# Kernel tuning notes

Hardware: AMD Instinct MI355X
Metric: run time of the kernel (lower is better)

The kernel has to match this reference:

```python
import jax, jax.numpy as jnp
import numpy as np

D_MODEL = 1024
H = 16
D_K = D_MODEL // H
D_FF = 4096
EPS = 1e-6
NEG = -1e9


def setup_inputs() -> dict:
    key = jax.random.key(0)
    ks = jax.random.split(key, 8)
    B, S = 2, 2048
    src = jax.random.normal(ks[0], (B, S, D_MODEL), dtype=jnp.float32)
    src_mask = jnp.ones((B, 1, 1, S), dtype=jnp.int32)
    sc = 1.0 / np.sqrt(D_MODEL)
    wq = jax.random.normal(ks[1], (D_MODEL, D_MODEL), jnp.float32) * sc
    wk = jax.random.normal(ks[2], (D_MODEL, D_MODEL), jnp.float32) * sc
    wv = jax.random.normal(ks[3], (D_MODEL, D_MODEL), jnp.float32) * sc
    wo = jax.random.normal(ks[4], (D_MODEL, D_MODEL), jnp.float32) * sc
    w1 = jax.random.normal(ks[5], (D_FF, D_MODEL), jnp.float32) * sc
    b1 = jnp.zeros((D_FF,), jnp.float32)
    w2 = jax.random.normal(ks[6], (D_MODEL, D_FF), jnp.float32) * (1.0 / np.sqrt(D_FF))
    b2 = jnp.zeros((D_MODEL,), jnp.float32)
    a1 = jnp.ones((1,), jnp.float32)
    be1 = jnp.zeros((1,), jnp.float32)
    a2 = jnp.ones((1,), jnp.float32)
    be2 = jnp.zeros((1,), jnp.float32)
    return dict(src=src, src_mask=src_mask, wq=wq, wk=wk, wv=wv, wo=wo,
                w1=w1, b1=b1, w2=w2, b2=b2, a1=a1, be1=be1, a2=a2, be2=be2)


def layer_norm(x, alpha, bias):
    # torch: mean + unbiased std (ddof=1), eps added to std
    mean = jnp.mean(x, axis=-1, keepdims=True)
    std = jnp.sqrt(jnp.var(x, axis=-1, keepdims=True, ddof=1))
    return alpha * (x - mean) / (std + EPS) + bias


def mha(x, mask, wq, wk, wv, wo):
    B, S, _ = x.shape
    def split(t):  # [B,S,D] -> [B,H,S,D_K]
        return t.reshape(B, S, H, D_K).transpose(0, 2, 1, 3)
    q = split(x @ wq.T)
    k = split(x @ wk.T)
    v = split(x @ wv.T)
    scores = jnp.einsum('bhqd,bhkd->bhqk', q, k) / np.sqrt(D_K)
    scores = jnp.where(mask == 0, NEG, scores)
    attn = jax.nn.softmax(scores, axis=-1)
    out = jnp.einsum('bhqk,bhkd->bhqd', attn, v)
    out = out.transpose(0, 2, 1, 3).reshape(B, S, D_MODEL)
    return out @ wo.T


def reference(src, src_mask, wq, wk, wv, wo, w1, b1, w2, b2, a1, be1, a2, be2):
    x = layer_norm(src, a1, be1)
    src = src + mha(x, src_mask, wq, wk, wv, wo)
    x = layer_norm(src, a2, be2)
    ff = jax.nn.relu(x @ w1.T + b1) @ w2.T + b2
    return src + ff
```

## Files before the change

### kernel.cpp

```cpp
#include <hip/hip_runtime.h>
#include <hip/hip_bf16.h>

typedef unsigned short u16;
typedef unsigned int u32;
typedef float floatx4 __attribute__((ext_vector_type(4)));
typedef __bf16 bf16x8 __attribute__((ext_vector_type(8)));
typedef u16 ushort4v __attribute__((ext_vector_type(4)));
typedef u16 ushort8v __attribute__((ext_vector_type(8)));
typedef u32 u32x2 __attribute__((ext_vector_type(2)));

#define DEVI static __device__ __forceinline__

DEVI u16 f2bf(float f) {
    u32 u = __builtin_bit_cast(u32, f);
    u += 0x7fffu + ((u >> 16) & 1u);
    return (u16)(u >> 16);
}
DEVI float bf2f(u16 h) { return __builtin_bit_cast(float, (u32)h << 16); }

DEVI float fexp2(float x) { return __builtin_amdgcn_exp2f(x); }

DEVI u32 cvtpk_bf16(float lo, float hi) {
    u32 r;
    asm("v_cvt_pk_bf16_f32 %0, %1, %2" : "=v"(r) : "v"(lo), "v"(hi));
    return r;
}

DEVI void async_cp16(const u16* g, u16* l) {
    __builtin_amdgcn_global_load_lds((const __attribute__((address_space(1))) u32*)g,
                                     (__attribute__((address_space(3))) u32*)l, 16, 0, 0);
}

template<int N> DEVI void wait_vmcnt() {
    if constexpr (N == 0)      asm volatile("s_waitcnt vmcnt(0)" ::: "memory");
    else if constexpr (N == 2) asm volatile("s_waitcnt vmcnt(2)" ::: "memory");
    else if constexpr (N == 3) asm volatile("s_waitcnt vmcnt(3)" ::: "memory");
    else if constexpr (N == 4) asm volatile("s_waitcnt vmcnt(4)" ::: "memory");
    else if constexpr (N == 6) asm volatile("s_waitcnt vmcnt(6)" ::: "memory");
    else static_assert(N == 0, "add vmcnt case");
}

#define PH_BAR() asm volatile("s_barrier" ::: "memory")

DEVI void xcd_swizzle(int& bx, int& by, int gx, int gy) {
    int L = by * gx + bx;
    int xcd = L & 7, s = L >> 3;
    int gh = gy >> 2, xh = gx >> 1;
    int mg = xcd & 3, ng = xcd >> 2;
    by = mg * gh + s % gh;
    bx = ng * xh + s / gh;
}

template<int BM, int BN, int RW, int CW, bool QKV3, int NSPLIT, bool XSWZ,
         bool BIAS, bool RELU, bool RESID, bool OBF16, bool VTW>
__global__ __launch_bounds__(256) void gemm_nt(
    const u16* __restrict__ A,
    const u16* __restrict__ W0, const u16* __restrict__ W1, const u16* __restrict__ W2,
    const float* __restrict__ bias, const float* __restrict__ resid,
    void* __restrict__ o0, void* __restrict__ o1, void* __restrict__ o2,
    void* __restrict__ o3, int K, int lda, int Nper, int NX)
{
    static_assert(RW * CW == 4, "4 waves");
    constexpr int WM = BM / RW, WN = BN / CW;
    constexpr int MI = WM / 16, NI = WN / 16;
    constexpr int LPT = BM / 64 + BN / 64;
    constexpr int ASZ = 3 * BM * 32;
    constexpr int BSZ = 3 * BN * 32;
    __shared__ __align__(16) u16 smem[ASZ + BSZ];
    u16* Asm = smem;
    u16* Bsm = smem + ASZ;
    const int tid = threadIdx.x;
    const int w = tid >> 6, lane = tid & 63;
    const int q = lane >> 4, ml = lane & 15;
    const int wr = w / CW, wc = w % CW;
    int bx = blockIdx.x, by = blockIdx.y;
    if (XSWZ) xcd_swizzle(bx, by, gridDim.x, gridDim.y);
    const int m0 = by * BM;
    size_t kbase = 0;
    const u16* W = W0;
    void* outp = o0;
    if (NSPLIT > 1) {
        int part = bx / NX; bx -= part * NX; kbase = (size_t)part * K;
        outp = (part == 0) ? o0 : (part == 1 ? o1 : (part == 2 ? o2 : o3));
    }
    int n0 = bx * BN;
    bool vwrite = false;
    if (QKV3) {
        int sel = n0 / Nper;
        n0 -= sel * Nper;
        W = (sel == 0) ? W0 : (sel == 1 ? W1 : W2);
        outp = (sel == 0) ? o0 : (sel == 1 ? o1 : o2);
        if (VTW) vwrite = (sel == 2);
    }

    auto stage = [&](int buf, int kt) {
#pragma unroll
        for (int p = 0; p < BM / 64; ++p) {
            int g = p * 256 + tid;
            int r = g >> 2, s = g & 3;
            int c = s ^ ((r >> 1) & 3);
            async_cp16(A + (size_t)(m0 + r) * lda + kbase + kt + c * 8,
                       &Asm[buf * (BM * 32) + (p * 256 + w * 64) * 8]);
        }
#pragma unroll
        for (int p = 0; p < BN / 64; ++p) {
            int g = p * 256 + tid;
            int r = g >> 2, s = g & 3;
            int c = s ^ ((r >> 1) & 3);
            async_cp16(W + (size_t)(n0 + r) * lda + kbase + kt + c * 8,
                       &Bsm[buf * (BN * 32) + (p * 256 + w * 64) * 8]);
        }
    };

    const floatx4 fzero = {0.f, 0.f, 0.f, 0.f};
    floatx4 acc[MI][NI];
#pragma unroll
    for (int i = 0; i < MI; ++i)
#pragma unroll
        for (int j = 0; j < NI; ++j) acc[i][j] = fzero;

    const int nt = K >> 5;
    stage(0, 0);
    stage(1, 32);
    int cb = 0, nb = 2;
    for (int it = 0, kt = 0; it < nt; ++it, kt += 32) {
        wait_vmcnt<LPT>();
        __builtin_amdgcn_s_barrier();
        __builtin_amdgcn_sched_barrier(0);
        int ktn = kt + 64; if (ktn > K - 32) ktn = K - 32;
        stage(nb, ktn);
        __builtin_amdgcn_sched_barrier(0);
        const u16* Asb = &Asm[cb * (BM * 32)];
        const u16* Bsb = &Bsm[cb * (BN * 32)];
        bf16x8 af[MI], bfr[NI];
#pragma unroll
        for (int i = 0; i < MI; ++i) {
            int rm = wr * WM + i * 16 + ml;
            int s = q ^ ((rm >> 1) & 3);
            af[i] = *(const bf16x8*)&Asb[(rm * 4 + s) * 8];
        }
#pragma unroll
        for (int j = 0; j < NI; ++j) {
            int rn = wc * WN + j * 16 + ml;
            int s = q ^ ((rn >> 1) & 3);
            bfr[j] = *(const bf16x8*)&Bsb[(rn * 4 + s) * 8];
        }
#pragma unroll
        for (int i = 0; i < MI; ++i)
#pragma unroll
            for (int j = 0; j < NI; ++j)
                acc[i][j] = __builtin_amdgcn_mfma_f32_16x16x32_bf16(af[i], bfr[j], acc[i][j], 0, 0, 0);
        cb = cb == 2 ? 0 : cb + 1;
        nb = nb == 2 ? 0 : nb + 1;
    }

    wait_vmcnt<0>();

    if constexpr (OBF16) {
        __builtin_amdgcn_s_barrier();
        char* T = (char*)smem;
        if (VTW && vwrite) {
#pragma unroll
            for (int j = 0; j < NI; ++j) {
                int nl = wc * WN + j * 16 + ml;
#pragma unroll
                for (int i = 0; i < MI; ++i) {
                    int m4 = wr * WM + i * 16 + q * 4;
                    u32x2 pk = {(u32)f2bf(acc[i][j][0]) | ((u32)f2bf(acc[i][j][1]) << 16),
                                (u32)f2bf(acc[i][j][2]) | ((u32)f2bf(acc[i][j][3]) << 16)};
                    *(u32x2*)(T + nl * (BM * 2) + ((m4 * 2) ^ ((nl & 15) << 4))) = pk;
                }
            }
            __syncthreads();
            const int bb = m0 >> 11, sres = m0 & 2047;
            constexpr int CPR = BM / 8, RPP = 256 / CPR;
#pragma unroll
            for (int p = 0; p < BN / RPP; ++p) {
                int nr = p * RPP + (tid / CPR);
                int c0 = (tid % CPR) * 8;
                bf16x8 vv = *(const bf16x8*)(T + nr * (BM * 2) + ((c0 * 2) ^ ((nr & 15) << 4)));
                *(bf16x8*)&((u16*)o3)[(size_t)(bb * 1024 + n0 + nr) * 2048 + sres + c0] = vv;
            }
        } else {
#pragma unroll
            for (int j = 0; j < NI; ++j) {
                int col = wc * WN + j * 16 + ml;
                float bj = 0.f;
                if (BIAS) bj = bias[n0 + col];
#pragma unroll
                for (int i = 0; i < MI; ++i) {
#pragma unroll
                    for (int r = 0; r < 4; ++r) {
                        int row = wr * WM + i * 16 + q * 4 + r;
                        float v = acc[i][j][r] + bj;
                        if (RELU) v = fmaxf(v, 0.f);
                        *(u16*)(T + row * (BN * 2) + ((col * 2) ^ ((row & 15) << 4))) = f2bf(v);
                    }
                }
            }
            __syncthreads();
            constexpr int CPR = BN / 8, RPP = 256 / CPR;
#pragma unroll
            for (int p = 0; p < BM / RPP; ++p) {
                int rr = p * RPP + (tid / CPR);
                int c0 = (tid % CPR) * 8;
                bf16x8 vv = *(const bf16x8*)(T + rr * (BN * 2) + ((c0 * 2) ^ ((rr & 15) << 4)));
                *(bf16x8*)&((u16*)outp)[(size_t)(m0 + rr) * Nper + n0 + c0] = vv;
            }
        }
    } else {
#pragma unroll
        for (int j = 0; j < NI; ++j) {
            int gn = n0 + wc * WN + j * 16 + ml;
            float bj = 0.f;
            if (BIAS) bj = bias[gn];
#pragma unroll
            for (int i = 0; i < MI; ++i) {
                int gm0 = m0 + wr * WM + i * 16 + q * 4;
#pragma unroll
                for (int r = 0; r < 4; ++r) {
                    size_t idx = (size_t)(gm0 + r) * Nper + gn;
                    float v = acc[i][j][r] + bj;
                    if (RELU) v = fmaxf(v, 0.f);
                    if (RESID) v += resid[idx];
                    ((float*)outp)[idx] = v;
                }
            }
        }
    }
}

template<bool QKV3, int NSPLIT, bool BIAS, bool RELU, bool VTW>
__global__ __launch_bounds__(512, 2) void gemm8p(
    const u16* __restrict__ A,
    const u16* __restrict__ W0, const u16* __restrict__ W1, const u16* __restrict__ W2,
    const float* __restrict__ bias,
    void* __restrict__ o0, void* __restrict__ o1, void* __restrict__ o2,
    void* __restrict__ o3, int K, int lda, int Nper, int NX)
{
    __shared__ __align__(16) u16 smem[65536];
    u16* Asm = smem;
    u16* Bsm = smem + 32768;
    const int tid = threadIdx.x;
    const int w = tid >> 6, lane = tid & 63;
    const int q = lane >> 4, ml = lane & 15;
    const int wr = w >> 2, wc = w & 3;
    int bx = blockIdx.x, by = blockIdx.y;
    xcd_swizzle(bx, by, gridDim.x, gridDim.y);
    const int m0 = by * 256;
    size_t kbase = 0;
    const u16* W = W0;
    void* outp = o0;
    if (NSPLIT > 1) {
        int part = bx / NX; bx -= part * NX; kbase = (size_t)part * K;
        outp = (part == 0) ? o0 : (part == 1 ? o1 : (part == 2 ? o2 : o3));
    }
    int n0 = bx * 256;
    if (QKV3) {
        int sel = n0 / Nper; n0 -= sel * Nper;
        W = (sel == 0) ? W0 : (sel == 1 ? W1 : W2);
        outp = (sel == 0) ? o0 : (sel == 1 ? o1 : o2);
    }

    auto stA = [&](int d, int kh, int kt) {
#pragma unroll
        for (int p = 0; p < 2; ++p) {
            int c = p * 512 + tid;
            int r = c >> 2;
            int sc = (c & 3) ^ ((r >> 1) & 3);
            async_cp16(A + (size_t)(m0 + r) * lda + kbase + kt + kh * 32 + sc * 8,
                       &Asm[(d * 2 + kh) * 8192 + (p * 512 + w * 64) * 8]);
        }
    };
    auto stB = [&](int d, int kh, int kt) {
#pragma unroll
        for (int p = 0; p < 2; ++p) {
            int c = p * 512 + tid;
            int r = c >> 2;
            int sc = (c & 3) ^ ((r >> 1) & 3);
            async_cp16(W + (size_t)(n0 + r) * lda + kbase + kt + kh * 32 + sc * 8,
                       &Bsm[(d * 2 + kh) * 8192 + (p * 512 + w * 64) * 8]);
        }
    };
    auto rdA = [&](int d, int kh, int i) -> bf16x8 {
        int rm = wr * 128 + i * 16 + ml;
        return *(const bf16x8*)&Asm[(d * 2 + kh) * 8192 + (rm * 4 + (q ^ ((rm >> 1) & 3))) * 8];
    };
    auto rdB = [&](int d, int kh, int j) -> bf16x8 {
        int rn = wc * 64 + j * 16 + ml;
        return *(const bf16x8*)&Bsm[(d * 2 + kh) * 8192 + (rn * 4 + (q ^ ((rn >> 1) & 3))) * 8];
    };

    const floatx4 fzero = {0.f, 0.f, 0.f, 0.f};
    floatx4 acc[8][4];
#pragma unroll
    for (int i = 0; i < 8; ++i)
#pragma unroll
        for (int j = 0; j < 4; ++j) acc[i][j] = fzero;

#define PHASE(d, kh, ih, STG, VM)                                              \
    {                                                                          \
        if (ih == 0) {                                                         \
            _Pragma("unroll")                                                  \
            for (int j = 0; j < 4; ++j) bfr[j] = rdB(d, kh, j);                \
        }                                                                      \
        _Pragma("unroll")                                                      \
        for (int ii = 0; ii < 4; ++ii) af[ii] = rdA(d, kh, (ih) * 4 + ii);     \
        STG;                                                                   \
        if (VM) wait_vmcnt<4>();                                               \
        PH_BAR();                                                              \
        __builtin_amdgcn_s_setprio(1);                                         \
        _Pragma("unroll")                                                      \
        for (int ii = 0; ii < 4; ++ii)                                         \
            _Pragma("unroll")                                                  \
            for (int j = 0; j < 4; ++j)                                        \
                acc[(ih) * 4 + ii][j] = __builtin_amdgcn_mfma_f32_16x16x32_bf16( \
                    af[ii], bfr[j], acc[(ih) * 4 + ii][j], 0, 0, 0);           \
        __builtin_amdgcn_s_setprio(0);                                         \
        PH_BAR();                                                              \
    }

    const int R = K >> 7;
    stA(0, 0, 0); stB(0, 0, 0); stA(0, 1, 0); stB(0, 1, 0);
    wait_vmcnt<0>();
    PH_BAR();

    for (int rr = 0; rr < R; ++rr) {
        const int kt1 = rr * 128 + 64;
        const int kt2 = (rr * 128 + 128 <= K - 64) ? rr * 128 + 128 : K - 64;
        bf16x8 af[4], bfr[4];
        PHASE(0, 0, 0, stA(1, 0, kt1), 0)
        PHASE(0, 0, 1, stB(1, 0, kt1), 1)
        PHASE(0, 1, 0, stA(1, 1, kt1), 0)
        PHASE(0, 1, 1, stB(1, 1, kt1), 1)
        PHASE(1, 0, 0, stA(0, 0, kt2), 0)
        PHASE(1, 0, 1, stB(0, 0, kt2), 1)
        PHASE(1, 1, 0, stA(0, 1, kt2), 0)
        PHASE(1, 1, 1, stB(0, 1, kt2), 1)
    }
#undef PHASE
    wait_vmcnt<0>();
    __builtin_amdgcn_s_barrier();

    char* T = (char*)smem;
#pragma unroll
    for (int j = 0; j < 4; ++j) {
        int col = wc * 64 + j * 16 + ml;
        float bj = 0.f;
        if (BIAS) bj = bias[n0 + col];
#pragma unroll
        for (int i = 0; i < 8; ++i) {
#pragma unroll
            for (int r = 0; r < 4; ++r) {
                int row = wr * 128 + i * 16 + q * 4 + r;
                float v = acc[i][j][r] + bj;
                if (RELU) v = fmaxf(v, 0.f);
                *(u16*)(T + row * 512 + ((col * 2) ^ ((row & 15) << 5))) = f2bf(v);
            }
        }
    }
    __syncthreads();
#pragma unroll
    for (int p = 0; p < 16; ++p) {
        int rr = p * 16 + (tid >> 5);
        int c0 = (tid & 31) * 8;
        bf16x8 vv = *(const bf16x8*)(T + rr * 512 + ((c0 * 2) ^ ((rr & 15) << 5)));
        *(bf16x8*)&((u16*)outp)[(size_t)(m0 + rr) * Nper + n0 + c0] = vv;
    }
}

__global__ __launch_bounds__(256, 2) void flash9(
    const u16* __restrict__ Q, const u16* __restrict__ Kg,
    const u16* __restrict__ Vt, const float* __restrict__ biasv,
    u16* __restrict__ O)
{
    __shared__ __align__(16) u16 smem[24576];
    const int tid = threadIdx.x;
    const int w = tid >> 6, lane = tid & 63;
    const int qw = w & 1, kv = w >> 1;
    const int q = lane >> 4, ml = lane & 15;
    int bx = blockIdx.x, by = blockIdx.y;
    {
        int L = by * 16 + bx;
        int xcd = L & 7, s = L >> 3;
        by = xcd * 4 + (s >> 4);
        bx = s & 15;
    }
    const int b = by >> 4, h = by & 15;
    const size_t rowQ = (size_t)(b * 2048 + bx * 128);
    const float KSC = 0.125f * 1.4426950408889634f;
    const floatx4 fzero = {0.f, 0.f, 0.f, 0.f};
    const ushort8v onesv = {0x3F80, 0x3F80, 0x3F80, 0x3F80,
                            0x3F80, 0x3F80, 0x3F80, 0x3F80};
    const bf16x8 vone = __builtin_bit_cast(bf16x8, onesv);

    bf16x8 qa[4][2];
#pragma unroll
    for (int qg = 0; qg < 4; ++qg)
#pragma unroll
        for (int c = 0; c < 2; ++c)
            qa[qg][c] = *(const bf16x8*)&Q[(rowQ + qw * 64 + qg * 16 + ml) * 1024
                                           + h * 64 + q * 8 + c * 32];

    auto stage = [&](int buf, int it) {
        {
            int row = tid >> 3, sl = tid & 7;
            int ch = sl ^ ((row & 3) | (((row >> 3) & 1) << 2));
#pragma unroll
            for (int hf = 0; hf < 2; ++hf)
                async_cp16(Kg + (size_t)(b * 2048 + hf * 1024 + it * 32 + row) * 1024
                               + h * 64 + ch * 8,
                           &smem[(hf * 3 + buf) * 2048 + w * 512]);
        }
        {
            int row = tid >> 2, sl = tid & 3;
            int ch = sl ^ ((row >> 1) & 3);
#pragma unroll
            for (int hf = 0; hf < 2; ++hf)
                async_cp16(Vt + (size_t)(b * 1024 + h * 64 + row) * 2048
                               + hf * 1024 + it * 32 + ch * 8,
                           &smem[12288 + (hf * 3 + buf) * 2048 + w * 512]);
        }
    };

    floatx4 oacc[4][4];
    floatx4 lacc[4];
#pragma unroll
    for (int qg = 0; qg < 4; ++qg) {
        lacc[qg] = fzero;
#pragma unroll
        for (int d = 0; d < 4; ++d) oacc[qg][d] = fzero;
    }

    const int swk = (ml & 3) | (((ml >> 2) & 1) << 2);
    const int re = ((ml >> 2) << 3) + (ml & 3);

    stage(0, 0);
    stage(1, 1);
    int cb = 0, nb = 2;
    for (int it = 0; it < 32; ++it) {
        asm volatile("s_waitcnt vmcnt(4)" ::: "memory");
        __builtin_amdgcn_s_barrier();
        __builtin_amdgcn_sched_barrier(0);
        const int s0 = kv * 1024 + it * 32;
        const float4 be = *(const float4*)&biasv[b * 2048 + s0 + q * 8];
        const float4 bo = *(const float4*)&biasv[b * 2048 + s0 + q * 8 + 4];
        __builtin_amdgcn_sched_barrier(0);
        stage(nb, it + 2 < 32 ? it + 2 : 31);

        const u16* Kb = &smem[(kv * 3 + cb) * 2048];
        const u16* Vb = &smem[12288 + (kv * 3 + cb) * 2048];

        bf16x8 ke0 = *(const bf16x8*)&Kb[(re + 0) * 64 + ((0 + q) ^ swk) * 8];
        bf16x8 ke1 = *(const bf16x8*)&Kb[(re + 0) * 64 + ((4 + q) ^ swk) * 8];
        bf16x8 ko0 = *(const bf16x8*)&Kb[(re + 4) * 64 + ((0 + q) ^ swk) * 8];
        bf16x8 ko1 = *(const bf16x8*)&Kb[(re + 4) * 64 + ((4 + q) ^ swk) * 8];
        bf16x8 pfrag[4];
#pragma unroll
        for (int qg = 0; qg < 4; ++qg) {
            floatx4 te = fzero, to = fzero;
            te = __builtin_amdgcn_mfma_f32_16x16x32_bf16(ke0, qa[qg][0], te, 0, 0, 0);
            te = __builtin_amdgcn_mfma_f32_16x16x32_bf16(ke1, qa[qg][1], te, 0, 0, 0);
            to = __builtin_amdgcn_mfma_f32_16x16x32_bf16(ko0, qa[qg][0], to, 0, 0, 0);
            to = __builtin_amdgcn_mfma_f32_16x16x32_bf16(ko1, qa[qg][1], to, 0, 0, 0);
            float pe0 = fexp2(fmaf(te[0], KSC, be.x));
            float pe1 = fexp2(fmaf(te[1], KSC, be.y));
            float pe2 = fexp2(fmaf(te[2], KSC, be.z));
            float pe3 = fexp2(fmaf(te[3], KSC, be.w));
            float po0 = fexp2(fmaf(to[0], KSC, bo.x));
            float po1 = fexp2(fmaf(to[1], KSC, bo.y));
            float po2 = fexp2(fmaf(to[2], KSC, bo.z));
            float po3 = fexp2(fmaf(to[3], KSC, bo.w));
            u32 pk[4];
            pk[0] = cvtpk_bf16(pe0, pe1);
            pk[1] = cvtpk_bf16(pe2, pe3);
            pk[2] = cvtpk_bf16(po0, po1);
            pk[3] = cvtpk_bf16(po2, po3);
            pfrag[qg] = __builtin_bit_cast(bf16x8, *(uint4*)pk);
            lacc[qg] = __builtin_amdgcn_mfma_f32_16x16x32_bf16(
                vone, pfrag[qg], lacc[qg], 0, 0, 0);
        }
#pragma unroll
        for (int dt = 0; dt < 4; ++dt) {
            int vrow = dt * 16 + ml;
            bf16x8 vf = *(const bf16x8*)&Vb[vrow * 32 + ((q ^ ((vrow >> 1) & 3)) * 8)];
#pragma unroll
            for (int qg = 0; qg < 4; ++qg)
                oacc[qg][dt] = __builtin_amdgcn_mfma_f32_16x16x32_bf16(
                    vf, pfrag[qg], oacc[qg][dt], 0, 0, 0);
        }
        cb = cb == 2 ? 0 : cb + 1;
        nb = nb == 2 ? 0 : nb + 1;
    }

    __syncthreads();
    float* sO = (float*)smem;
    float* sL = (float*)smem + 8192;
    if (kv == 1) {
#pragma unroll
        for (int qg = 0; qg < 4; ++qg) {
            sL[(qw * 4 + qg) * 64 + lane] = lacc[qg][0];
#pragma unroll
            for (int dt = 0; dt < 4; ++dt)
                *(floatx4*)&sO[((qw * 4 + qg) * 4 + dt) * 256 + lane * 4] = oacc[qg][dt];
        }
    }
    __syncthreads();
    if (kv == 1) return;
#pragma unroll
    for (int qg = 0; qg < 4; ++qg) {
        float ls = lacc[qg][0] + sL[(qw * 4 + qg) * 64 + lane];
#pragma unroll
        for (int dt = 0; dt < 4; ++dt)
            oacc[qg][dt] += *(const floatx4*)&sO[((qw * 4 + qg) * 4 + dt) * 256 + lane * 4];
        const float rcp = 1.f / ls;
        const size_t row = rowQ + qw * 64 + qg * 16 + ml;
#pragma unroll
        for (int dt = 0; dt < 4; ++dt)
#pragma unroll
            for (int rp = 0; rp < 4; rp += 2) {
                u32 pk = (u32)f2bf(oacc[qg][dt][rp] * rcp)
                       | ((u32)f2bf(oacc[qg][dt][rp + 1] * rcp) << 16);
                *(u32*)&O[row * 1024 + h * 64 + dt * 16 + q * 4 + rp] = pk;
            }
    }
}

DEVI void ln_row(const float* __restrict__ x, float ga, float gb,
                 u16* __restrict__ y, int row, int tid)
{
    const float4 v = ((const float4*)(x + (size_t)row * 1024))[tid];
    float s = v.x + v.y + v.z + v.w;
    float ss = v.x * v.x + v.y * v.y + v.z * v.z + v.w * v.w;
#pragma unroll
    for (int d = 1; d < 64; d <<= 1) { s += __shfl_xor(s, d, 64); ss += __shfl_xor(ss, d, 64); }
    __shared__ float ps[4], pss[4];
    const int w = tid >> 6, lane = tid & 63;
    if (lane == 0) { ps[w] = s; pss[w] = ss; }
    __syncthreads();
    s = ps[0] + ps[1] + ps[2] + ps[3];
    ss = pss[0] + pss[1] + pss[2] + pss[3];
    float mean = s * (1.f / 1024.f);
    float var = fmaxf((ss - s * mean) * (1.f / 1023.f), 0.f);
    float sc = ga / (sqrtf(var) + 1e-6f);
    ushort4v o;
    o[0] = f2bf((v.x - mean) * sc + gb);
    o[1] = f2bf((v.y - mean) * sc + gb);
    o[2] = f2bf((v.z - mean) * sc + gb);
    o[3] = f2bf((v.w - mean) * sc + gb);
    ((ushort4v*)(y + (size_t)row * 1024))[tid] = o;
}

__global__ __launch_bounds__(256) void ln_bf16(const float* __restrict__ x,
    const float* __restrict__ ga, const float* __restrict__ gb, u16* __restrict__ y)
{
    ln_row(x, ga[0], gb[0], y, blockIdx.x, threadIdx.x);
}

__global__ __launch_bounds__(256) void prep(
    const float* __restrict__ wq, const float* __restrict__ wk,
    const float* __restrict__ wv, const float* __restrict__ wo,
    const float* __restrict__ w1, const float* __restrict__ w2,
    u16* __restrict__ wqb, u16* __restrict__ wkb, u16* __restrict__ wvb,
    u16* __restrict__ wob, u16* __restrict__ w1b, u16* __restrict__ w2b,
    const int* __restrict__ m, float* __restrict__ biasv,
    const float* __restrict__ src, const float* __restrict__ a1,
    const float* __restrict__ be1, u16* __restrict__ xln1)
{
    const int bx = blockIdx.x;
    if (bx < 12288) {
        size_t i = (size_t)bx * 256 + threadIdx.x;
        const float* s; u16* d; size_t off;
        if (i < 262144)       { s = wq; d = wqb; off = i; }
        else if (i < 524288)  { s = wk; d = wkb; off = i - 262144; }
        else if (i < 786432)  { s = wv; d = wvb; off = i - 524288; }
        else if (i < 1048576) { s = wo; d = wob; off = i - 786432; }
        else if (i < 2097152) { s = w1; d = w1b; off = i - 1048576; }
        else                  { s = w2; d = w2b; off = i - 2097152; }
        float4 v = ((const float4*)s)[off];
        ushort4v o = {f2bf(v.x), f2bf(v.y), f2bf(v.z), f2bf(v.w)};
        ((ushort4v*)d)[off] = o;
    } else if (bx < 12304) {
        int i = (bx - 12288) * 256 + threadIdx.x;
        biasv[i] = m[i] ? 0.f : -1.442695e9f;
    } else {
        ln_row(src, a1[0], be1[0], xln1, bx - 12304, threadIdx.x);
    }
}

__global__ __launch_bounds__(256) void ff2_fin(
    const u16* __restrict__ p0, const u16* __restrict__ p1,
    const u16* __restrict__ p2, const u16* __restrict__ p3,
    const float* __restrict__ b2, const float* __restrict__ resid,
    float* __restrict__ out)
{
    const size_t i = (size_t)blockIdx.x * 256 + threadIdx.x;
    ushort4v a = *(const ushort4v*)&p0[i * 4];
    ushort4v b = *(const ushort4v*)&p1[i * 4];
    ushort4v c = *(const ushort4v*)&p2[i * 4];
    ushort4v d = *(const ushort4v*)&p3[i * 4];
    float4 r = ((const float4*)resid)[i];
    float4 bb = ((const float4*)b2)[i & 255];
    float4 o;
    o.x = ((bf2f(a[0]) + bf2f(b[0])) + (bf2f(c[0]) + bf2f(d[0]))) + r.x + bb.x;
    o.y = ((bf2f(a[1]) + bf2f(b[1])) + (bf2f(c[1]) + bf2f(d[1]))) + r.y + bb.y;
    o.z = ((bf2f(a[2]) + bf2f(b[2])) + (bf2f(c[2]) + bf2f(d[2]))) + r.z + bb.z;
    o.w = ((bf2f(a[3]) + bf2f(b[3])) + (bf2f(c[3]) + bf2f(d[3]))) + r.w + bb.w;
    ((float4*)out)[i] = o;
}

extern "C" void kernel_launch(void* const* d_in, const int* in_sizes, int n_in,
                              void* d_out, int out_size, void* d_ws, size_t ws_size,
                              hipStream_t stream)
{
    const float* src = (const float*)d_in[0];
    const int* msk   = (const int*)d_in[1];
    const float* wq  = (const float*)d_in[2];
    const float* wk  = (const float*)d_in[3];
    const float* wv  = (const float*)d_in[4];
    const float* wo  = (const float*)d_in[5];
    const float* w1  = (const float*)d_in[6];
    const float* b1  = (const float*)d_in[7];
    const float* w2  = (const float*)d_in[8];
    const float* b2  = (const float*)d_in[9];
    const float* a1  = (const float*)d_in[10];
    const float* be1 = (const float*)d_in[11];
    const float* a2  = (const float*)d_in[12];
    const float* be2 = (const float*)d_in[13];
    float* out = (float*)d_out;

    char* ws = (char*)d_ws;
    const size_t MB = (size_t)1 << 20;
    u16* wqb  = (u16*)(ws + 0 * MB);
    u16* wkb  = (u16*)(ws + 2 * MB);
    u16* wvb  = (u16*)(ws + 4 * MB);
    u16* wob  = (u16*)(ws + 6 * MB);
    u16* w1b  = (u16*)(ws + 8 * MB);
    u16* w2b  = (u16*)(ws + 16 * MB);
    u16* xln1 = (u16*)(ws + 24 * MB);
    u16* attn = xln1;
    u16* Qb   = (u16*)(ws + 32 * MB);
    u16* xln2 = Qb;
    u16* Kb   = (u16*)(ws + 40 * MB);
    u16* Vt   = (u16*)(ws + 56 * MB);
    float* biasv = (float*)(ws + 64 * MB);
    u16* h1   = (u16*)(ws + 40 * MB);
    float* src2 = (float*)(ws + 72 * MB);
    u16* P0 = (u16*)(ws + 0 * MB);
    u16* P1 = (u16*)(ws + 8 * MB);
    u16* P2 = (u16*)(ws + 24 * MB);
    u16* P3 = (u16*)(ws + 32 * MB);

    prep<<<16400, 256, 0, stream>>>(wq, wk, wv, wo, w1, w2,
                                    wqb, wkb, wvb, wob, w1b, w2b,
                                    msk, biasv, src, a1, be1, xln1);

    gemm_nt<128, 128, 2, 2, true, 1, true, false, false, false, true, true><<<dim3(24, 32), 256, 0, stream>>>(
        xln1, wqb, wkb, wvb, nullptr, nullptr, Qb, Kb, nullptr, Vt, 1024, 1024, 1024, 0);

    flash9<<<dim3(16, 32), 256, 0, stream>>>(Qb, Kb, Vt, biasv, attn);

    gemm_nt<128, 64, 4, 1, false, 1, true, false, false, true, false, false><<<dim3(16, 32), 256, 0, stream>>>(
        attn, wob, nullptr, nullptr, nullptr, src, src2, nullptr, nullptr, nullptr,
        1024, 1024, 1024, 0);

    ln_bf16<<<4096, 256, 0, stream>>>(src2, a2, be2, xln2);

    gemm8p<false, 1, true, true, false><<<dim3(16, 16), 512, 0, stream>>>(
        xln2, w1b, nullptr, nullptr, b1, h1, nullptr, nullptr, nullptr,
        1024, 1024, 4096, 0);

    gemm8p<false, 4, false, false, false><<<dim3(16, 16), 512, 0, stream>>>(
        h1, w2b, nullptr, nullptr, nullptr, P0, P1, P2, P3,
        1024, 4096, 1024, 4);

    ff2_fin<<<4096, 256, 0, stream>>>(P0, P1, P2, P3, b2, src2, out);
}
```

Before: 316.3 us.

## Replace 8-phase FFN GEMM pipeline with triple-buffered K32 loop and new swizzles

Rewrites the 256x256 FFN GEMM kernel's main loop. The 8-phase, double-buffered, two-half-K64 schedule with two barriers per phase becomes a simpler triple-buffered K=32 loop: one barrier per step, with the prefetch issued two steps ahead. It also changes the XCD block swizzle to give each XCD a contiguous band of M rows, and changes the epilogue LDS XOR swizzle to use row bits 2-3. The aim is fewer barriers and better L2 locality per XCD. The trade-off is less MFMA work per barrier, which could expose more latency.

```diff
diff --git a/kernel.cpp b/kernel.cpp
--- a/kernel.cpp
+++ b/kernel.cpp
@@ -40,15 +40,12 @@
     else static_assert(N == 0, "add vmcnt case");
 }
 
-#define PH_BAR() asm volatile("s_barrier" ::: "memory")
-
 DEVI void xcd_swizzle(int& bx, int& by, int gx, int gy) {
     int L = by * gx + bx;
     int xcd = L & 7, s = L >> 3;
-    int gh = gy >> 2, xh = gx >> 1;
-    int mg = xcd & 3, ng = xcd >> 2;
-    by = mg * gh + s % gh;
-    bx = ng * xh + s / gh;
+    int mb = gy >> 3;
+    by = xcd * mb + s % mb;
+    bx = s / mb;
 }
 
 template<int BM, int BN, int RW, int CW, bool QKV3, int NSPLIT, bool XSWZ,
@@ -194,7 +191,7 @@
                         int row = wr * WM + i * 16 + q * 4 + r;
                         float v = acc[i][j][r] + bj;
                         if (RELU) v = fmaxf(v, 0.f);
-                        *(u16*)(T + row * (BN * 2) + ((col * 2) ^ ((row & 15) << 4))) = f2bf(v);
+                        *(u16*)(T + row * (BN * 2) + ((col * 2) ^ (((row >> 2) & 3) << 5))) = f2bf(v);
                     }
                 }
             }
@@ -204,7 +201,7 @@
             for (int p = 0; p < BM / RPP; ++p) {
                 int rr = p * RPP + (tid / CPR);
                 int c0 = (tid % CPR) * 8;
-                bf16x8 vv = *(const bf16x8*)(T + rr * (BN * 2) + ((c0 * 2) ^ ((rr & 15) << 4)));
+                bf16x8 vv = *(const bf16x8*)(T + rr * (BN * 2) + ((c0 * 2) ^ (((rr >> 2) & 3) << 5)));
                 *(bf16x8*)&((u16*)outp)[(size_t)(m0 + rr) * Nper + n0 + c0] = vv;
             }
         }
@@ -230,17 +227,16 @@
     }
 }
 
-template<bool QKV3, int NSPLIT, bool BIAS, bool RELU, bool VTW>
-__global__ __launch_bounds__(512, 2) void gemm8p(
-    const u16* __restrict__ A,
-    const u16* __restrict__ W0, const u16* __restrict__ W1, const u16* __restrict__ W2,
+template<int NSPLIT, bool BIAS, bool RELU>
+__global__ __launch_bounds__(512, 2) void gemm256(
+    const u16* __restrict__ A, const u16* __restrict__ W0,
     const float* __restrict__ bias,
     void* __restrict__ o0, void* __restrict__ o1, void* __restrict__ o2,
     void* __restrict__ o3, int K, int lda, int Nper, int NX)
 {
     __shared__ __align__(16) u16 smem[65536];
     u16* Asm = smem;
-    u16* Bsm = smem + 32768;
+    u16* Bsm = smem + 24576;
     const int tid = threadIdx.x;
     const int w = tid >> 6, lane = tid & 63;
     const int q = lane >> 4, ml = lane & 15;
@@ -249,46 +245,30 @@
     xcd_swizzle(bx, by, gridDim.x, gridDim.y);
     const int m0 = by * 256;
     size_t kbase = 0;
-    const u16* W = W0;
     void* outp = o0;
     if (NSPLIT > 1) {
         int part = bx / NX; bx -= part * NX; kbase = (size_t)part * K;
         outp = (part == 0) ? o0 : (part == 1 ? o1 : (part == 2 ? o2 : o3));
     }
-    int n0 = bx * 256;
-    if (QKV3) {
-        int sel = n0 / Nper; n0 -= sel * Nper;
-        W = (sel == 0) ? W0 : (sel == 1 ? W1 : W2);
-        outp = (sel == 0) ? o0 : (sel == 1 ? o1 : o2);
-    }
-
-    auto stA = [&](int d, int kh, int kt) {
+    const int n0 = bx * 256;
+
+    auto stage = [&](int buf, int kt) {
 #pragma unroll
         for (int p = 0; p < 2; ++p) {
             int c = p * 512 + tid;
             int r = c >> 2;
             int sc = (c & 3) ^ ((r >> 1) & 3);
-            async_cp16(A + (size_t)(m0 + r) * lda + kbase + kt + kh * 32 + sc * 8,
-                       &Asm[(d * 2 + kh) * 8192 + (p * 512 + w * 64) * 8]);
-        }
-    };
-    auto stB = [&](int d, int kh, int kt) {
+            async_cp16(A + (size_t)(m0 + r) * lda + kbase + kt + sc * 8,
+                       &Asm[buf * 8192 + (p * 512 + w * 64) * 8]);
+        }
 #pragma unroll
         for (int p = 0; p < 2; ++p) {
             int c = p * 512 + tid;
             int r = c >> 2;
             int sc = (c & 3) ^ ((r >> 1) & 3);
-            async_cp16(W + (size_t)(n0 + r) * lda + kbase + kt + kh * 32 + sc * 8,
-                       &Bsm[(d * 2 + kh) * 8192 + (p * 512 + w * 64) * 8]);
-        }
-    };
-    auto rdA = [&](int d, int kh, int i) -> bf16x8 {
-        int rm = wr * 128 + i * 16 + ml;
-        return *(const bf16x8*)&Asm[(d * 2 + kh) * 8192 + (rm * 4 + (q ^ ((rm >> 1) & 3))) * 8];
-    };
-    auto rdB = [&](int d, int kh, int j) -> bf16x8 {
-        int rn = wc * 64 + j * 16 + ml;
-        return *(const bf16x8*)&Bsm[(d * 2 + kh) * 8192 + (rn * 4 + (q ^ ((rn >> 1) & 3))) * 8];
+            async_cp16(W0 + (size_t)(n0 + r) * lda + kbase + kt + sc * 8,
+                       &Bsm[buf * 8192 + (p * 512 + w * 64) * 8]);
+        }
     };
 
     const floatx4 fzero = {0.f, 0.f, 0.f, 0.f};
@@ -298,47 +278,41 @@
 #pragma unroll
         for (int j = 0; j < 4; ++j) acc[i][j] = fzero;
 
-#define PHASE(d, kh, ih, STG, VM)                                              \
-    {                                                                          \
-        if (ih == 0) {                                                         \
-            _Pragma("unroll")                                                  \
-            for (int j = 0; j < 4; ++j) bfr[j] = rdB(d, kh, j);                \
-        }                                                                      \
-        _Pragma("unroll")                                                      \
-        for (int ii = 0; ii < 4; ++ii) af[ii] = rdA(d, kh, (ih) * 4 + ii);     \
-        STG;                                                                   \
-        if (VM) wait_vmcnt<4>();                                               \
-        PH_BAR();                                                              \
-        __builtin_amdgcn_s_setprio(1);                                         \
-        _Pragma("unroll")                                                      \
-        for (int ii = 0; ii < 4; ++ii)                                         \
-            _Pragma("unroll")                                                  \
-            for (int j = 0; j < 4; ++j)                                        \
-                acc[(ih) * 4 + ii][j] = __builtin_amdgcn_mfma_f32_16x16x32_bf16( \
-                    af[ii], bfr[j], acc[(ih) * 4 + ii][j], 0, 0, 0);           \
-        __builtin_amdgcn_s_setprio(0);                                         \
-        PH_BAR();                                                              \
-    }
-
-    const int R = K >> 7;
-    stA(0, 0, 0); stB(0, 0, 0); stA(0, 1, 0); stB(0, 1, 0);
-    wait_vmcnt<0>();
-    PH_BAR();
-
-    for (int rr = 0; rr < R; ++rr) {
-        const int kt1 = rr * 128 + 64;
-        const int kt2 = (rr * 128 + 128 <= K - 64) ? rr * 128 + 128 : K - 64;
-        bf16x8 af[4], bfr[4];
-        PHASE(0, 0, 0, stA(1, 0, kt1), 0)
-        PHASE(0, 0, 1, stB(1, 0, kt1), 1)
-        PHASE(0, 1, 0, stA(1, 1, kt1), 0)
-        PHASE(0, 1, 1, stB(1, 1, kt1), 1)
-        PHASE(1, 0, 0, stA(0, 0, kt2), 0)
-        PHASE(1, 0, 1, stB(0, 0, kt2), 1)
-        PHASE(1, 1, 0, stA(0, 1, kt2), 0)
-        PHASE(1, 1, 1, stB(0, 1, kt2), 1)
-    }
-#undef PHASE
+    const int nt = K >> 5;
+    stage(0, 0);
+    stage(1, 32);
+    int cb = 0, nb = 2;
+    for (int it = 0, kt = 0; it < nt; ++it, kt += 32) {
+        wait_vmcnt<4>();
+        __builtin_amdgcn_s_barrier();
+        __builtin_amdgcn_sched_barrier(0);
+        int ktn = kt + 64; if (ktn > K - 32) ktn = K - 32;
+        stage(nb, ktn);
+        __builtin_amdgcn_sched_barrier(0);
+        const u16* Asb = &Asm[cb * 8192];
+        const u16* Bsb = &Bsm[cb * 8192];
+        bf16x8 af[8], bfr[4];
+#pragma unroll
+        for (int i = 0; i < 8; ++i) {
+            int rm = wr * 128 + i * 16 + ml;
+            af[i] = *(const bf16x8*)&Asb[(rm * 4 + (q ^ ((rm >> 1) & 3))) * 8];
+        }
+#pragma unroll
+        for (int j = 0; j < 4; ++j) {
+            int rn = wc * 64 + j * 16 + ml;
+            bfr[j] = *(const bf16x8*)&Bsb[(rn * 4 + (q ^ ((rn >> 1) & 3))) * 8];
+        }
+        __builtin_amdgcn_s_setprio(1);
+#pragma unroll
+        for (int i = 0; i < 8; ++i)
+#pragma unroll
+            for (int j = 0; j < 4; ++j)
+                acc[i][j] = __builtin_amdgcn_mfma_f32_16x16x32_bf16(af[i], bfr[j], acc[i][j], 0, 0, 0);
+        __builtin_amdgcn_s_setprio(0);
+        cb = cb == 2 ? 0 : cb + 1;
+        nb = nb == 2 ? 0 : nb + 1;
+    }
+
     wait_vmcnt<0>();
     __builtin_amdgcn_s_barrier();
 
@@ -355,7 +329,7 @@
                 int row = wr * 128 + i * 16 + q * 4 + r;
                 float v = acc[i][j][r] + bj;
                 if (RELU) v = fmaxf(v, 0.f);
-                *(u16*)(T + row * 512 + ((col * 2) ^ ((row & 15) << 5))) = f2bf(v);
+                *(u16*)(T + row * 512 + ((col * 2) ^ (((row >> 2) & 3) << 5))) = f2bf(v);
             }
         }
     }
@@ -364,7 +338,7 @@
     for (int p = 0; p < 16; ++p) {
         int rr = p * 16 + (tid >> 5);
         int c0 = (tid & 31) * 8;
-        bf16x8 vv = *(const bf16x8*)(T + rr * 512 + ((c0 * 2) ^ ((rr & 15) << 5)));
+        bf16x8 vv = *(const bf16x8*)(T + rr * 512 + ((c0 * 2) ^ (((rr >> 2) & 3) << 5)));
         *(bf16x8*)&((u16*)outp)[(size_t)(m0 + rr) * Nper + n0 + c0] = vv;
     }
 }
@@ -666,13 +640,11 @@
 
     ln_bf16<<<4096, 256, 0, stream>>>(src2, a2, be2, xln2);
 
-    gemm8p<false, 1, true, true, false><<<dim3(16, 16), 512, 0, stream>>>(
-        xln2, w1b, nullptr, nullptr, b1, h1, nullptr, nullptr, nullptr,
-        1024, 1024, 4096, 0);
-
-    gemm8p<false, 4, false, false, false><<<dim3(16, 16), 512, 0, stream>>>(
-        h1, w2b, nullptr, nullptr, nullptr, P0, P1, P2, P3,
-        1024, 4096, 1024, 4);
+    gemm256<1, true, true><<<dim3(16, 16), 512, 0, stream>>>(
+        xln2, w1b, b1, h1, nullptr, nullptr, nullptr, 1024, 1024, 4096, 0);
+
+    gemm256<4, false, false><<<dim3(16, 16), 512, 0, stream>>>(
+        h1, w2b, nullptr, P0, P1, P2, P3, 1024, 4096, 1024, 4);
 
     ff2_fin<<<4096, 256, 0, stream>>>(P0, P1, P2, P3, b2, src2, out);
 }
```

New measurement: 304.7 us. 3.7% less time.
